# Kernel optimization log

Measured on AMD Instinct MI355X. Metric: run time of the kernel, lower is better.

Reference implementation:

```python
import jax, jax.numpy as jnp
import numpy as np
from jax.scipy.special import logsumexp

EPS_SINK = 0.1
N_ITERS = 100
LN_EPS = 1e-5
ANAT_W = (1.0, 1.0, 1.2)  # anatomical_weights[0:3] used by _get_region_weights
GRIDS = ((5, 0.2), (15, 0.3), (25, 0.5))  # (grid_size, scale_weight)


def layernorm(x, g, b):
    m = x.mean(-1, keepdims=True)
    v = ((x - m) ** 2).mean(-1, keepdims=True)
    return (x - m) / jnp.sqrt(v + LN_EPS) * g + b


def spatial_distribution(bb, g):
    # bb: [B, D, 4] in 0..1000 coords -> [B, D, g*g] binary occupancy grid
    B, D, _ = bb.shape
    bc = bb * (g / 1000.0)
    x, y, w, h = bc[..., 0], bc[..., 1], bc[..., 2], bc[..., 3]
    x1 = jnp.maximum(jnp.trunc(x), 0.0)          # max(0, int(x))
    y1 = jnp.maximum(jnp.trunc(y), 0.0)
    x2 = jnp.minimum(jnp.trunc(x + w), g - 1.0)  # min(g-1, int(x+w))
    y2 = jnp.minimum(jnp.trunc(y + h), g - 1.0)
    gi = jnp.arange(g, dtype=bb.dtype)
    row = (gi[None, None, :, None] >= y1[..., None, None]) & (gi[None, None, :, None] <= y2[..., None, None])
    col = (gi[None, None, None, :] >= x1[..., None, None]) & (gi[None, None, None, :] <= x2[..., None, None])
    nz = jnp.any(bc != 0, axis=-1)[..., None, None]
    grid = (row & col & nz).astype(bb.dtype)  # [B, D, g, g]
    return grid.reshape(B, D, g * g)


def emd_pairs(d1, d2, g):
    # d1, d2: [B, P, n] spatial distributions; returns [B, P] pseudo-EMD exactly as source
    yy, xx = jnp.meshgrid(jnp.arange(g), jnp.arange(g), indexing='ij')
    pos = jnp.stack([xx.ravel(), yy.ravel()], axis=1).astype(jnp.float32)
    diff = pos[:, None, :] - pos[None, :, :]
    C = jnp.sqrt((diff * diff).sum(-1))
    C = C / C.max()
    rw = jnp.ones((g, g), jnp.float32)
    rw = rw.at[: g // 3].mul(ANAT_W[0]).at[g // 3 : (2 * g) // 3].mul(ANAT_W[1]).at[(2 * g) // 3 :].mul(ANAT_W[2])
    C = C * rw.ravel()  # broadcast over columns, same as torch C[n,n] * weights[n]
    K = jnp.exp(-C / EPS_SINK)
    logP = jnp.log(d1[..., :, None] + 1e-8)  # [B,P,n,1]
    logQ = jnp.log(d2[..., None, :] + 1e-8)  # [B,P,1,n]

    def step(carry, _):
        u, v = carry
        u = logP - logsumexp(v + K, axis=-1, keepdims=True)
        v = logQ - logsumexp(u + K.T, axis=-2, keepdims=True)
        return (u, v), None

    (u, v), _ = jax.lax.scan(step, (jnp.zeros_like(logP), jnp.zeros_like(logQ)), None, length=N_ITERS)
    Pm = jnp.exp(u + v + K)
    return (Pm * C).sum((-2, -1))


def setup_inputs() -> dict:
    key = jax.random.key(0)
    ks = jax.random.split(key, 6)
    B, D, F, Hd = 1, 14, 768, 256
    features = jax.random.normal(ks[0], (B, D, F), jnp.float32)
    # x,y in [0,800), w,h in [0,200) so boxes stay inside the 0..1000 frame
    bb = jax.random.uniform(ks[1], (B, D, 4), jnp.float32) * jnp.array([800.0, 800.0, 200.0, 200.0])
    return {
        'features': features,
        'bb_coords': bb,
        'w_embed': jax.random.normal(ks[2], (F, Hd), jnp.float32) * 0.02,
        'b_embed': jnp.zeros((Hd,), jnp.float32),
        'g1': jnp.ones((Hd,), jnp.float32),
        'b1': jnp.zeros((Hd,), jnp.float32),
        'gat_W': jax.random.normal(ks[3], (3, Hd, Hd), jnp.float32) * 0.02,
        'gat_b': jnp.zeros((3, Hd), jnp.float32),
        'gat_g': jnp.ones((3, Hd), jnp.float32),
        'gat_bt': jnp.zeros((3, Hd), jnp.float32),
        'w_out': jax.random.normal(ks[4], (Hd, F), jnp.float32) * 0.02,
        'b_out': jnp.zeros((F,), jnp.float32),
        'g2': jnp.ones((F,), jnp.float32),
        'b2': jnp.zeros((F,), jnp.float32),
    }


def reference(features, bb_coords, w_embed, b_embed, g1, b1, gat_W, gat_b, gat_g, gat_bt, w_out, b_out, g2, b2):
    B, D, _ = features.shape
    H = 1  # num_heads (the only shape-consistent value for the source module)
    x = layernorm(features @ w_embed + b_embed, g1, b1)

    # --- EMD-based adjacency over all 91 unordered disease pairs, vectorized ---
    iu, ju = np.triu_indices(D, k=1)
    adj = jnp.zeros((B, D, D), features.dtype)
    for g, sw in GRIDS:
        dist = spatial_distribution(bb_coords, g)            # [B, D, g*g]
        emd = emd_pairs(dist[:, iu], dist[:, ju], g)         # [B, 91]
        adj = adj.at[:, iu, ju].add(sw * emd).at[:, ju, iu].add(sw * emd)
    adj = jax.nn.softmax(adj, axis=-1)

    # --- 3 GAT layers (q=k=v, per source) ---
    attns = []
    for l in range(3):
        h = x @ gat_W[l] + gat_b[l]                          # [B, D, 256]
        hd = h.shape[-1] // H
        q = h.reshape(B, D, H, hd).transpose(0, 2, 1, 3)     # [B, H, D, hd]
        attn = jnp.einsum('bhnd,bhmd->bhnm', q, q) * hd ** -0.5
        attn = jnp.where(adj[:, None] == 0, -jnp.inf, attn)
        attn = jax.nn.softmax(attn, axis=-1)
        o = jnp.einsum('bhnm,bhmd->bhnd', attn, q)
        o = o.transpose(0, 2, 1, 3).reshape(B, D, H * hd)
        x = layernorm(o, gat_g[l], gat_bt[l])
        attns.append(attn.mean(1))
        x = jax.nn.elu(x)

    out = layernorm(x @ w_out + b_out, g2, b2)
    final_attention = jnp.stack(attns).mean(0)
    return out, final_attention
```

## Files before the change

kernel.cpp:

```cpp
#include <hip/hip_runtime.h>
#include <math.h>


#define NWG 16

__device__ __forceinline__ void astore(float* p, float v) {
  __hip_atomic_store(p, v, __ATOMIC_RELAXED, __HIP_MEMORY_SCOPE_AGENT);
}

__device__ __forceinline__ void bar_arrive(int* bar, int slot) {
  asm volatile("s_waitcnt vmcnt(0)" ::: "memory");
  __syncthreads();
  if (threadIdx.x == 0)
    __hip_atomic_fetch_add(&bar[slot], 1, __ATOMIC_RELAXED,
                           __HIP_MEMORY_SCOPE_AGENT);
}

__device__ __forceinline__ void bar_wait(int* bar, int slot) {
  if (threadIdx.x == 0) {
    while (__hip_atomic_load(&bar[slot], __ATOMIC_RELAXED,
                             __HIP_MEMORY_SCOPE_AGENT) < NWG)
      __builtin_amdgcn_s_sleep(1);
  }
  __syncthreads();
  asm volatile("" ::: "memory");
}

__device__ __forceinline__ void row_stats(const float* Xs, float* Pb,
                                          float* Mn, float* Rs, int tid) {
  if (tid < 224) {
    const int r = tid >> 4, seg = tid & 15;
    const float* p = Xs + r * 260 + seg * 16;
    const float4 a = *(const float4*)(p);
    const float4 b = *(const float4*)(p + 4);
    const float4 c = *(const float4*)(p + 8);
    const float4 d = *(const float4*)(p + 12);
    Pb[tid] = (((a.x + a.y) + (a.z + a.w)) + ((b.x + b.y) + (b.z + b.w))) +
              (((c.x + c.y) + (c.z + c.w)) + ((d.x + d.y) + (d.z + d.w)));
  }
  __syncthreads();
  if (tid < 14) {
    float s = 0.f;
#pragma unroll
    for (int q = 0; q < 16; ++q) s += Pb[tid * 16 + q];
    Mn[tid] = s * (1.f / 256.f);
  }
  __syncthreads();
  if (tid < 224) {
    const int r = tid >> 4, seg = tid & 15;
    const float m = Mn[r];
    const float* p = Xs + r * 260 + seg * 16;
    float s = 0.f;
#pragma unroll
    for (int i = 0; i < 16; ++i) {
      const float dv = p[i] - m;
      s = fmaf(dv, dv, s);
    }
    Pb[tid] = s;
  }
  __syncthreads();
  if (tid < 14) {
    float s = 0.f;
#pragma unroll
    for (int q = 0; q < 16; ++q) s += Pb[tid * 16 + q];
    Rs[tid] = rsqrtf(s * (1.f / 256.f) + 1e-5f);
  }
  __syncthreads();
}

__global__ __launch_bounds__(1024) void sdg_fused(
    const float* __restrict__ feat, const float* __restrict__ w_embed,
    const float* __restrict__ b_embed, const float* __restrict__ g1,
    const float* __restrict__ b1, const float* __restrict__ gat_W,
    const float* __restrict__ gat_b, const float* __restrict__ gat_g,
    const float* __restrict__ gat_bt, const float* __restrict__ w_out,
    const float* __restrict__ b_out, const float* __restrict__ g2,
    const float* __restrict__ b2, float* __restrict__ out, int* bar,
    float* __restrict__ e_ws, float* __restrict__ h_ws,
    float* __restrict__ gp_ws, float* __restrict__ st1_ws,
    float* __restrict__ st2_ws) {
  const int w = blockIdx.x, tid = threadIdx.x;
  const int w16 = w * 16, w48 = w * 48;
  const int c = tid & 15;
  const int ksl = (tid >> 4) & 15;
  const int rg = tid >> 8;

  __shared__ __align__(16) float SA[14592];
  __shared__ __align__(16) float SB[10752];
  __shared__ __align__(16) float Pb[3600];
  __shared__ float Hb[240];
  __shared__ float Asm[224];
  __shared__ float aRow[224];
  __shared__ float Ov[686];
  __shared__ float Mn[14], Rs[14], ps[14], psq[14];

  float* const Fs = SB;
  float* const Xs = SB;
  float* const Ht = SB + 3640;

#pragma unroll
  for (int i = 0; i < 3; ++i) {
    const int idx = i * 1024 + tid;
    const int k = idx >> 2, q = (idx & 3) * 4;
    const float4 v = *(const float4*)(&w_embed[k * 256 + w16 + q]);
    SA[k * 19 + q + 0] = v.x;
    SA[k * 19 + q + 1] = v.y;
    SA[k * 19 + q + 2] = v.z;
    SA[k * 19 + q + 3] = v.w;
  }
  for (int i = tid; i < 2688; i += 1024)
    *(float4*)(&Fs[i * 4]) = ((const float4*)feat)[i];
  if (tid < 224) aRow[tid] = 0.f;
  if (tid < 28) Asm[(tid >> 1) * 16 + 14 + (tid & 1)] = 0.f;
  __syncthreads();

  {
    float acc[4] = {0.f, 0.f, 0.f, 0.f};
    const int r0 = rg * 4, kb = ksl * 48;
#pragma unroll
    for (int ch = 0; ch < 12; ++ch) {
      const int k = kb + ch * 4;
      const float w0 = SA[(k + 0) * 19 + c];
      const float w1 = SA[(k + 1) * 19 + c];
      const float w2 = SA[(k + 2) * 19 + c];
      const float w3 = SA[(k + 3) * 19 + c];
#pragma unroll
      for (int rr = 0; rr < 4; ++rr) {
        const int r = r0 + rr;
        if (r < 14) {
          const float4 xv = *(const float4*)(&Fs[r * 768 + k]);
          acc[rr] = fmaf(
              xv.x, w0,
              fmaf(xv.y, w1, fmaf(xv.z, w2, fmaf(xv.w, w3, acc[rr]))));
        }
      }
    }
#pragma unroll
    for (int rr = 0; rr < 4; ++rr) {
      const int r = r0 + rr;
      if (r < 14) Pb[ksl * 225 + r * 16 + c] = acc[rr];
    }
  }
  __syncthreads();
  if (tid < 224) {
    const int r = tid >> 4, cc = tid & 15;
    float v = b_embed[w16 + cc];
#pragma unroll
    for (int q = 0; q < 16; ++q) v += Pb[q * 225 + tid];
    astore(&e_ws[r * 256 + w16 + cc], v);
    float sv = v, sq = v * v;
#pragma unroll
    for (int off = 8; off; off >>= 1) {
      sv += __shfl_xor(sv, off, 16);
      sq += __shfl_xor(sq, off, 16);
    }
    if (cc == 0) {
      astore(&st1_ws[w * 28 + r], sv);
      astore(&st1_ws[w * 28 + 14 + r], sq);
    }
  }
  bar_arrive(bar, 0);
  {
    const int k = tid >> 2, q = (tid & 3) * 4;
    const float4 v = *(const float4*)(&gat_W[k * 256 + w16 + q]);
    SA[k * 19 + q + 0] = v.x;
    SA[k * 19 + q + 1] = v.y;
    SA[k * 19 + q + 2] = v.z;
    SA[k * 19 + q + 3] = v.w;
  }
  bar_wait(bar, 0);

  if (tid < 14) {
    float S = 0.f, Q = 0.f;
#pragma unroll
    for (int q = 0; q < 16; ++q) {
      S += st1_ws[q * 28 + tid];
      Q += st1_ws[q * 28 + 14 + tid];
    }
    const float m = S * (1.f / 256.f);
    Mn[tid] = m;
    Rs[tid] = rsqrtf(Q * (1.f / 256.f) - m * m + 1e-5f);
    ps[tid] = 0.f;
    psq[tid] = 0.f;
  }
  if (tid < 896) {
    const float4 v = ((const float4*)e_ws)[tid];
    const int idx = tid * 4, r = idx >> 8, cc = idx & 255;
    *(float4*)(&Xs[r * 260 + cc]) = v;
  }
  if (tid < 520) Ht[14 * 260 + tid] = 0.f;
  __syncthreads();
  for (int i = tid; i < 3584; i += 1024) {
    const int r = i >> 8, cc = i & 255;
    Xs[r * 260 + cc] = (Xs[r * 260 + cc] - Mn[r]) * Rs[r] * g1[cc] + b1[cc];
  }
  __syncthreads();

  for (int l = 0; l < 3; ++l) {
    {
      float acc[4] = {0.f, 0.f, 0.f, 0.f};
      const int r0 = rg * 4, kb = ksl * 16;
#pragma unroll
      for (int ch = 0; ch < 4; ++ch) {
        const int k = kb + ch * 4;
        const float w0 = SA[(k + 0) * 19 + c];
        const float w1 = SA[(k + 1) * 19 + c];
        const float w2 = SA[(k + 2) * 19 + c];
        const float w3 = SA[(k + 3) * 19 + c];
#pragma unroll
        for (int rr = 0; rr < 4; ++rr) {
          const int r = r0 + rr;
          if (r < 14) {
            const float4 xv = *(const float4*)(&Xs[r * 260 + k]);
            acc[rr] = fmaf(
                xv.x, w0,
                fmaf(xv.y, w1, fmaf(xv.z, w2, fmaf(xv.w, w3, acc[rr]))));
          }
        }
      }
#pragma unroll
      for (int rr = 0; rr < 4; ++rr) {
        const int r = r0 + rr;
        if (r < 14) Pb[ksl * 225 + r * 16 + c] = acc[rr];
      }
    }
    __syncthreads();
    if (tid < 224) {
      const int r = tid >> 4, cc = tid & 15;
      float v = gat_b[l * 256 + w16 + cc];
#pragma unroll
      for (int q = 0; q < 16; ++q) v += Pb[q * 225 + tid];
      Hb[r * 17 + cc] = v;
      astore(&h_ws[l * 3584 + r * 256 + w16 + cc], v);
    }
    __syncthreads();
    if (tid < 196) {
      const int i = tid / 14, j = tid - i * 14;
      float s = 0.f;
#pragma unroll
      for (int cc = 0; cc < 16; ++cc)
        s = fmaf(Hb[i * 17 + cc], Hb[j * 17 + cc], s);
      astore(&gp_ws[l * 3328 + w * 208 + tid], s);
    }
    bar_arrive(bar, 1 + l);
    if (l < 2) {
      const float* Wn = gat_W + (l + 1) * 65536;
      const int k = tid >> 2, q = (tid & 3) * 4;
      const float4 v = *(const float4*)(&Wn[k * 256 + w16 + q]);
      SA[k * 19 + q + 0] = v.x;
      SA[k * 19 + q + 1] = v.y;
      SA[k * 19 + q + 2] = v.z;
      SA[k * 19 + q + 3] = v.w;
    } else {
#pragma unroll
      for (int g = 0; g < 3; ++g) {
        const int k = tid >> 2, q = (tid & 3) * 4;
        const float4 v = *(const float4*)(&w_out[k * 768 + w48 + g * 16 + q]);
        SA[g * 4864 + k * 19 + q + 0] = v.x;
        SA[g * 4864 + k * 19 + q + 1] = v.y;
        SA[g * 4864 + k * 19 + q + 2] = v.z;
        SA[g * 4864 + k * 19 + q + 3] = v.w;
      }
    }
    bar_wait(bar, 1 + l);

    float glog = 0.f;
    if (tid < 196) {
      const float* gpl = gp_ws + l * 3328 + tid;
#pragma unroll
      for (int ww = 0; ww < 16; ++ww) glog += gpl[ww * 208];
    }
    if (tid < 896) {
      const float4 v = ((const float4*)(h_ws + l * 3584))[tid];
      const int idx = tid * 4, r = idx >> 8, cc = idx & 255;
      *(float4*)(&Ht[r * 260 + cc]) = v;
    }
    if (tid < 196) {
      const int i = tid / 14, j = tid - i * 14;
      Asm[i * 16 + j] = glog * 0.0625f;
    }
    __syncthreads();
    if (tid < 224) {
      const int r = tid >> 4, j = tid & 15;
      const float lv = (j < 14) ? Asm[r * 16 + j] : -1e30f;
      float mx = lv;
#pragma unroll
      for (int off = 8; off; off >>= 1) mx = fmaxf(mx, __shfl_xor(mx, off, 16));
      float p = (j < 14) ? expf(lv - mx) : 0.f;
      float sm = p;
#pragma unroll
      for (int off = 8; off; off >>= 1) sm += __shfl_xor(sm, off, 16);
      p /= sm;
      if (j < 14) {
        Asm[r * 16 + j] = p;
        aRow[r * 16 + j] += p * (1.f / 3.f);
      }
    }
    __syncthreads();
    if (l == 2 && w < 14 && tid < 14)
      out[10752 + w * 14 + tid] = aRow[w * 16 + tid];
    const int t2 = tid & 255;
    float o[4] = {0.f, 0.f, 0.f, 0.f};
#pragma unroll
    for (int mc = 0; mc < 4; ++mc) {
      const float v0 = Ht[(mc * 4 + 0) * 260 + t2];
      const float v1 = Ht[(mc * 4 + 1) * 260 + t2];
      const float v2 = Ht[(mc * 4 + 2) * 260 + t2];
      const float v3 = Ht[(mc * 4 + 3) * 260 + t2];
#pragma unroll
      for (int rr = 0; rr < 4; ++rr) {
        const int r = rg * 4 + rr;
        if (r < 14) {
          const float4 a = *(const float4*)(&Asm[r * 16 + mc * 4]);
          o[rr] =
              fmaf(a.x, v0, fmaf(a.y, v1, fmaf(a.z, v2, fmaf(a.w, v3, o[rr]))));
        }
      }
    }
#pragma unroll
    for (int rr = 0; rr < 4; ++rr) {
      const int r = rg * 4 + rr;
      if (r < 14) Xs[r * 260 + t2] = o[rr];
    }
    __syncthreads();
    row_stats(Xs, Pb, Mn, Rs, tid);
    {
      const float gc = gat_g[l * 256 + t2], bc = gat_bt[l * 256 + t2];
#pragma unroll
      for (int rr = 0; rr < 4; ++rr) {
        const int r = rg * 4 + rr;
        if (r < 14) {
          const float xn = (o[rr] - Mn[r]) * Rs[r] * gc + bc;
          Xs[r * 260 + t2] = xn > 0.f ? xn : expm1f(xn);
        }
      }
    }
    __syncthreads();
  }

  for (int g = 0; g < 3; ++g) {
    {
      float acc[4] = {0.f, 0.f, 0.f, 0.f};
      const int r0 = rg * 4, kb = ksl * 16;
#pragma unroll
      for (int ch = 0; ch < 4; ++ch) {
        const int k = kb + ch * 4;
        const float w0 = SA[g * 4864 + (k + 0) * 19 + c];
        const float w1 = SA[g * 4864 + (k + 1) * 19 + c];
        const float w2 = SA[g * 4864 + (k + 2) * 19 + c];
        const float w3 = SA[g * 4864 + (k + 3) * 19 + c];
#pragma unroll
        for (int rr = 0; rr < 4; ++rr) {
          const int r = r0 + rr;
          if (r < 14) {
            const float4 xv = *(const float4*)(&Xs[r * 260 + k]);
            acc[rr] = fmaf(
                xv.x, w0,
                fmaf(xv.y, w1, fmaf(xv.z, w2, fmaf(xv.w, w3, acc[rr]))));
          }
        }
      }
#pragma unroll
      for (int rr = 0; rr < 4; ++rr) {
        const int r = r0 + rr;
        if (r < 14) Pb[ksl * 225 + r * 16 + c] = acc[rr];
      }
    }
    __syncthreads();
    if (tid < 224) {
      const int r = tid >> 4, cc = tid & 15;
      float v = b_out[w48 + g * 16 + cc];
#pragma unroll
      for (int q = 0; q < 16; ++q) v += Pb[q * 225 + tid];
      Ov[r * 49 + g * 16 + cc] = v;
      float sv = v, sq = v * v;
#pragma unroll
      for (int off = 8; off; off >>= 1) {
        sv += __shfl_xor(sv, off, 16);
        sq += __shfl_xor(sq, off, 16);
      }
      if (cc == 0) {
        ps[r] += sv;
        psq[r] += sq;
      }
    }
    __syncthreads();
  }
  if (tid < 14) {
    astore(&st2_ws[w * 28 + tid], ps[tid]);
    astore(&st2_ws[w * 28 + 14 + tid], psq[tid]);
  }
  bar_arrive(bar, 4);
  bar_wait(bar, 4);
  if (tid < 14) {
    float S = 0.f, Q = 0.f;
#pragma unroll
    for (int q = 0; q < 16; ++q) {
      S += st2_ws[q * 28 + tid];
      Q += st2_ws[q * 28 + 14 + tid];
    }
    const float m = S * (1.f / 768.f);
    Mn[tid] = m;
    Rs[tid] = rsqrtf(Q * (1.f / 768.f) - m * m + 1e-5f);
  }
  __syncthreads();
  if (tid < 224) {
    const int r = tid >> 4, cc = tid & 15;
    const float m = Mn[r], rs = Rs[r];
#pragma unroll
    for (int g = 0; g < 3; ++g) {
      const int col = w48 + g * 16 + cc;
      out[r * 768 + col] = (Ov[r * 49 + g * 16 + cc] - m) * rs * g2[col] +
                           b2[col];
    }
  }
}

extern "C" void kernel_launch(void* const* d_in, const int* in_sizes, int n_in,
                              void* d_out, int out_size, void* d_ws,
                              size_t ws_size, hipStream_t stream) {
  const float* feat = (const float*)d_in[0];
  const float* w_embed = (const float*)d_in[2];
  const float* b_embed = (const float*)d_in[3];
  const float* g1 = (const float*)d_in[4];
  const float* b1 = (const float*)d_in[5];
  const float* gat_W = (const float*)d_in[6];
  const float* gat_b = (const float*)d_in[7];
  const float* gat_g = (const float*)d_in[8];
  const float* gat_bt = (const float*)d_in[9];
  const float* w_out = (const float*)d_in[10];
  const float* b_out = (const float*)d_in[11];
  const float* g2 = (const float*)d_in[12];
  const float* b2 = (const float*)d_in[13];
  float* out = (float*)d_out;

  int* bar = (int*)d_ws;
  float* e_ws = (float*)d_ws + 16;
  float* h_ws = e_ws + 3584;
  float* gp_ws = h_ws + 3 * 3584;
  float* st1_ws = gp_ws + 3 * 3328;
  float* st2_ws = st1_ws + 448;

  hipMemsetAsync(bar, 0, 16 * sizeof(int), stream);
  sdg_fused<<<NWG, 1024, 0, stream>>>(feat, w_embed, b_embed, g1, b1, gat_W,
                                      gat_b, gat_g, gat_bt, w_out, b_out, g2,
                                      b2, out, bar, e_ws, h_ws, gp_ws, st1_ws,
                                      st2_ws);
}
```

Baseline: 40.62 us.

## Compute GAT layernorm stats algebraically from Gram matrix and column sums

Replaces the per-layer row_stats pass (four barrier-separated shared-memory reductions over the attention output) with closed-form statistics. The mean comes from attention weights times per-node h sums, and the variance from A·G·Aᵀ using the already-reduced global Gram matrix. Each workgroup now also publishes per-row h sums alongside the Gram partials. h is read straight from global into registers instead of being staged in shared memory, and the cross-WG stat reductions now use 16-lane shuffles. The trade is fewer block syncs for a few more global reads, with the variance now computed as E[x²]−m², which risks precision loss through cancellation.

```diff
diff --git a/kernel.cpp b/kernel.cpp
--- a/kernel.cpp
+++ b/kernel.cpp
@@ -24,48 +24,6 @@
   }
   __syncthreads();
   asm volatile("" ::: "memory");
-}
-
-__device__ __forceinline__ void row_stats(const float* Xs, float* Pb,
-                                          float* Mn, float* Rs, int tid) {
-  if (tid < 224) {
-    const int r = tid >> 4, seg = tid & 15;
-    const float* p = Xs + r * 260 + seg * 16;
-    const float4 a = *(const float4*)(p);
-    const float4 b = *(const float4*)(p + 4);
-    const float4 c = *(const float4*)(p + 8);
-    const float4 d = *(const float4*)(p + 12);
-    Pb[tid] = (((a.x + a.y) + (a.z + a.w)) + ((b.x + b.y) + (b.z + b.w))) +
-              (((c.x + c.y) + (c.z + c.w)) + ((d.x + d.y) + (d.z + d.w)));
-  }
-  __syncthreads();
-  if (tid < 14) {
-    float s = 0.f;
-#pragma unroll
-    for (int q = 0; q < 16; ++q) s += Pb[tid * 16 + q];
-    Mn[tid] = s * (1.f / 256.f);
-  }
-  __syncthreads();
-  if (tid < 224) {
-    const int r = tid >> 4, seg = tid & 15;
-    const float m = Mn[r];
-    const float* p = Xs + r * 260 + seg * 16;
-    float s = 0.f;
-#pragma unroll
-    for (int i = 0; i < 16; ++i) {
-      const float dv = p[i] - m;
-      s = fmaf(dv, dv, s);
-    }
-    Pb[tid] = s;
-  }
-  __syncthreads();
-  if (tid < 14) {
-    float s = 0.f;
-#pragma unroll
-    for (int q = 0; q < 16; ++q) s += Pb[tid * 16 + q];
-    Rs[tid] = rsqrtf(s * (1.f / 256.f) + 1e-5f);
-  }
-  __syncthreads();
 }
 
 __global__ __launch_bounds__(1024) void sdg_fused(
@@ -84,19 +42,21 @@
   const int c = tid & 15;
   const int ksl = (tid >> 4) & 15;
   const int rg = tid >> 8;
+  const int t2 = tid & 255;
 
   __shared__ __align__(16) float SA[14592];
   __shared__ __align__(16) float SB[10752];
   __shared__ __align__(16) float Pb[3600];
   __shared__ float Hb[240];
+  __shared__ float Gm[224];
   __shared__ float Asm[224];
   __shared__ float aRow[224];
+  __shared__ float hm[16];
   __shared__ float Ov[686];
   __shared__ float Mn[14], Rs[14], ps[14], psq[14];
 
   float* const Fs = SB;
   float* const Xs = SB;
-  float* const Ht = SB + 3640;
 
 #pragma unroll
   for (int i = 0; i < 3; ++i) {
@@ -112,6 +72,7 @@
     *(float4*)(&Fs[i * 4]) = ((const float4*)feat)[i];
   if (tid < 224) aRow[tid] = 0.f;
   if (tid < 28) Asm[(tid >> 1) * 16 + 14 + (tid & 1)] = 0.f;
+  if (tid < 2) hm[14 + tid] = 0.f;
   __syncthreads();
 
   {
@@ -130,8 +91,7 @@
         if (r < 14) {
           const float4 xv = *(const float4*)(&Fs[r * 768 + k]);
           acc[rr] = fmaf(
-              xv.x, w0,
-              fmaf(xv.y, w1, fmaf(xv.z, w2, fmaf(xv.w, w3, acc[rr]))));
+              xv.x, w0, fmaf(xv.y, w1, fmaf(xv.z, w2, fmaf(xv.w, w3, acc[rr]))));
         }
       }
     }
@@ -170,25 +130,26 @@
   }
   bar_wait(bar, 0);
 
-  if (tid < 14) {
-    float S = 0.f, Q = 0.f;
-#pragma unroll
-    for (int q = 0; q < 16; ++q) {
-      S += st1_ws[q * 28 + tid];
-      Q += st1_ws[q * 28 + 14 + tid];
-    }
-    const float m = S * (1.f / 256.f);
-    Mn[tid] = m;
-    Rs[tid] = rsqrtf(Q * (1.f / 256.f) - m * m + 1e-5f);
-    ps[tid] = 0.f;
-    psq[tid] = 0.f;
+  if (tid < 224) {
+    const int r = tid >> 4, seg = tid & 15;
+    float S = st1_ws[seg * 28 + r];
+    float Q = st1_ws[seg * 28 + 14 + r];
+#pragma unroll
+    for (int off = 8; off; off >>= 1) {
+      S += __shfl_xor(S, off, 16);
+      Q += __shfl_xor(Q, off, 16);
+    }
+    if (seg == 0) {
+      const float m = S * (1.f / 256.f);
+      Mn[r] = m;
+      Rs[r] = rsqrtf(Q * (1.f / 256.f) - m * m + 1e-5f);
+    }
   }
   if (tid < 896) {
     const float4 v = ((const float4*)e_ws)[tid];
     const int idx = tid * 4, r = idx >> 8, cc = idx & 255;
     *(float4*)(&Xs[r * 260 + cc]) = v;
   }
-  if (tid < 520) Ht[14 * 260 + tid] = 0.f;
   __syncthreads();
   for (int i = tid; i < 3584; i += 1024) {
     const int r = i >> 8, cc = i & 255;
@@ -232,6 +193,10 @@
       for (int q = 0; q < 16; ++q) v += Pb[q * 225 + tid];
       Hb[r * 17 + cc] = v;
       astore(&h_ws[l * 3584 + r * 256 + w16 + cc], v);
+      float sv = v;
+#pragma unroll
+      for (int off = 8; off; off >>= 1) sv += __shfl_xor(sv, off, 16);
+      if (cc == 0) astore(&gp_ws[l * 3584 + w * 224 + 196 + r], sv);
     }
     __syncthreads();
     if (tid < 196) {
@@ -240,7 +205,7 @@
 #pragma unroll
       for (int cc = 0; cc < 16; ++cc)
         s = fmaf(Hb[i * 17 + cc], Hb[j * 17 + cc], s);
-      astore(&gp_ws[l * 3328 + w * 208 + tid], s);
+      astore(&gp_ws[l * 3584 + w * 224 + tid], s);
     }
     bar_arrive(bar, 1 + l);
     if (l < 2) {
@@ -264,20 +229,26 @@
     }
     bar_wait(bar, 1 + l);
 
-    float glog = 0.f;
+    float hv[16];
+    hv[14] = 0.f;
+    hv[15] = 0.f;
+#pragma unroll
+    for (int m = 0; m < 14; ++m) hv[m] = h_ws[l * 3584 + m * 256 + t2];
     if (tid < 196) {
-      const float* gpl = gp_ws + l * 3328 + tid;
-#pragma unroll
-      for (int ww = 0; ww < 16; ++ww) glog += gpl[ww * 208];
-    }
-    if (tid < 896) {
-      const float4 v = ((const float4*)(h_ws + l * 3584))[tid];
-      const int idx = tid * 4, r = idx >> 8, cc = idx & 255;
-      *(float4*)(&Ht[r * 260 + cc]) = v;
-    }
-    if (tid < 196) {
+      float s = 0.f;
+      const float* gpl = gp_ws + l * 3584 + tid;
+#pragma unroll
+      for (int ww = 0; ww < 16; ++ww) s += gpl[ww * 224];
       const int i = tid / 14, j = tid - i * 14;
-      Asm[i * 16 + j] = glog * 0.0625f;
+      Gm[i * 16 + j] = s;
+      Asm[i * 16 + j] = s * 0.0625f;
+    } else if (tid < 210) {
+      const int m = tid - 196;
+      float s = 0.f;
+      const float* gpl = gp_ws + l * 3584 + 196 + m;
+#pragma unroll
+      for (int ww = 0; ww < 16; ++ww) s += gpl[ww * 224];
+      hm[m] = s * (1.f / 256.f);
     }
     __syncthreads();
     if (tid < 224) {
@@ -297,33 +268,43 @@
       }
     }
     __syncthreads();
-    if (l == 2 && w < 14 && tid < 14)
-      out[10752 + w * 14 + tid] = aRow[w * 16 + tid];
-    const int t2 = tid & 255;
     float o[4] = {0.f, 0.f, 0.f, 0.f};
 #pragma unroll
     for (int mc = 0; mc < 4; ++mc) {
-      const float v0 = Ht[(mc * 4 + 0) * 260 + t2];
-      const float v1 = Ht[(mc * 4 + 1) * 260 + t2];
-      const float v2 = Ht[(mc * 4 + 2) * 260 + t2];
-      const float v3 = Ht[(mc * 4 + 3) * 260 + t2];
 #pragma unroll
       for (int rr = 0; rr < 4; ++rr) {
         const int r = rg * 4 + rr;
         if (r < 14) {
           const float4 a = *(const float4*)(&Asm[r * 16 + mc * 4]);
-          o[rr] =
-              fmaf(a.x, v0, fmaf(a.y, v1, fmaf(a.z, v2, fmaf(a.w, v3, o[rr]))));
-        }
-      }
-    }
-#pragma unroll
-    for (int rr = 0; rr < 4; ++rr) {
-      const int r = rg * 4 + rr;
-      if (r < 14) Xs[r * 260 + t2] = o[rr];
-    }
-    __syncthreads();
-    row_stats(Xs, Pb, Mn, Rs, tid);
+          o[rr] = fmaf(a.x, hv[mc * 4 + 0],
+                       fmaf(a.y, hv[mc * 4 + 1],
+                            fmaf(a.z, hv[mc * 4 + 2],
+                                 fmaf(a.w, hv[mc * 4 + 3], o[rr]))));
+        }
+      }
+    }
+    if (tid < 224) {
+      const int r = tid >> 4, j = tid & 15;
+      const float aj = Asm[r * 16 + j];
+      float tq = 0.f;
+      if (j < 14) {
+#pragma unroll
+        for (int i = 0; i < 14; ++i)
+          tq = fmaf(Asm[r * 16 + i], Gm[i * 16 + j], tq);
+      }
+      float qv = tq * aj;
+      float mv = aj * hm[j];
+#pragma unroll
+      for (int off = 8; off; off >>= 1) {
+        qv += __shfl_xor(qv, off, 16);
+        mv += __shfl_xor(mv, off, 16);
+      }
+      if (j == 0) {
+        Mn[r] = mv;
+        Rs[r] = rsqrtf(qv * (1.f / 256.f) - mv * mv + 1e-5f);
+      }
+    }
+    __syncthreads();
     {
       const float gc = gat_g[l * 256 + t2], bc = gat_bt[l * 256 + t2];
 #pragma unroll
@@ -332,6 +313,14 @@
         if (r < 14) {
           const float xn = (o[rr] - Mn[r]) * Rs[r] * gc + bc;
           Xs[r * 260 + t2] = xn > 0.f ? xn : expm1f(xn);
+        }
+      }
+      if (l == 2) {
+        if (w < 14 && tid < 14)
+          out[10752 + w * 14 + tid] = aRow[w * 16 + tid];
+        if (tid < 14) {
+          ps[tid] = 0.f;
+          psq[tid] = 0.f;
         }
       }
     }
@@ -392,16 +381,20 @@
   }
   bar_arrive(bar, 4);
   bar_wait(bar, 4);
-  if (tid < 14) {
-    float S = 0.f, Q = 0.f;
-#pragma unroll
-    for (int q = 0; q < 16; ++q) {
-      S += st2_ws[q * 28 + tid];
-      Q += st2_ws[q * 28 + 14 + tid];
-    }
-    const float m = S * (1.f / 768.f);
-    Mn[tid] = m;
-    Rs[tid] = rsqrtf(Q * (1.f / 768.f) - m * m + 1e-5f);
+  if (tid < 224) {
+    const int r = tid >> 4, seg = tid & 15;
+    float S = st2_ws[seg * 28 + r];
+    float Q = st2_ws[seg * 28 + 14 + r];
+#pragma unroll
+    for (int off = 8; off; off >>= 1) {
+      S += __shfl_xor(S, off, 16);
+      Q += __shfl_xor(Q, off, 16);
+    }
+    if (seg == 0) {
+      const float m = S * (1.f / 768.f);
+      Mn[r] = m;
+      Rs[r] = rsqrtf(Q * (1.f / 768.f) - m * m + 1e-5f);
+    }
   }
   __syncthreads();
   if (tid < 224) {
@@ -410,8 +403,8 @@
 #pragma unroll
     for (int g = 0; g < 3; ++g) {
       const int col = w48 + g * 16 + cc;
-      out[r * 768 + col] = (Ov[r * 49 + g * 16 + cc] - m) * rs * g2[col] +
-                           b2[col];
+      out[r * 768 + col] =
+          (Ov[r * 49 + g * 16 + cc] - m) * rs * g2[col] + b2[col];
     }
   }
 }
@@ -438,7 +431,7 @@
   float* e_ws = (float*)d_ws + 16;
   float* h_ws = e_ws + 3584;
   float* gp_ws = h_ws + 3 * 3584;
-  float* st1_ws = gp_ws + 3 * 3328;
+  float* st1_ws = gp_ws + 3 * 3584;
   float* st2_ws = st1_ws + 448;
 
   hipMemsetAsync(bar, 0, 16 * sizeof(int), stream);
```

Result: no change. 40.33 us (-0.7%).
